# Optimization experiments

Measured on AMD Instinct MI355X. Metric: run time of the kernel, lower is better.

The kernel has to match this reference:

```python
import jax, jax.numpy as jnp
import numpy as np

B, S, W = 8, 1024, 512          # batch, bert seq len, max word num
D, H, F, L, V = 768, 12, 3072, 4, 28996
CH = 512                         # BERT_MAX_LEN chunk size
EPS = 1e-12

def _ln(x, g, b):
    mu = x.mean(-1, keepdims=True)
    var = ((x - mu) ** 2).mean(-1, keepdims=True)
    return (x - mu) / jnp.sqrt(var + EPS) * g + b

def setup_inputs() -> dict:
    key = jax.random.key(0)
    ks = jax.random.split(key, 32)
    s = 0.02
    inp = {}
    inp['x_bert'] = jax.random.randint(ks[0], (B, S), 0, V)
    inp['x_bert_mask'] = jnp.ones((B, S), jnp.float32)
    bnd = jnp.sort(jax.random.randint(ks[1], (B, W + 1), 0, S + 1), axis=1)
    inp['x_bert_offset'] = jnp.stack([bnd[:, :-1], bnd[:, 1:]], axis=-1)  # [B,W,2], st<=ed
    inp['x_mask'] = jax.random.randint(ks[2], (B, W), 0, 2).astype(jnp.int32)
    inp['word_emb'] = jax.random.normal(ks[3], (V, D), jnp.float32) * s
    inp['pos_emb'] = jax.random.normal(ks[4], (CH, D), jnp.float32) * s
    inp['type_emb'] = jax.random.normal(ks[5], (2, D), jnp.float32) * s
    inp['emb_g'] = jnp.ones((D,), jnp.float32); inp['emb_b'] = jnp.zeros((D,), jnp.float32)
    inp['Wq'] = jax.random.normal(ks[6], (L, D, D), jnp.float32) * s
    inp['bq'] = jnp.zeros((L, D), jnp.float32)
    inp['Wk'] = jax.random.normal(ks[7], (L, D, D), jnp.float32) * s
    inp['bk'] = jnp.zeros((L, D), jnp.float32)
    inp['Wv'] = jax.random.normal(ks[8], (L, D, D), jnp.float32) * s
    inp['bv'] = jnp.zeros((L, D), jnp.float32)
    inp['Wo'] = jax.random.normal(ks[9], (L, D, D), jnp.float32) * s
    inp['bo'] = jnp.zeros((L, D), jnp.float32)
    inp['ln1_g'] = jnp.ones((L, D), jnp.float32); inp['ln1_b'] = jnp.zeros((L, D), jnp.float32)
    inp['W1'] = jax.random.normal(ks[10], (L, D, F), jnp.float32) * s
    inp['b1f'] = jnp.zeros((L, F), jnp.float32)
    inp['W2'] = jax.random.normal(ks[11], (L, F, D), jnp.float32) * s
    inp['b2f'] = jnp.zeros((L, D), jnp.float32)
    inp['ln2_g'] = jnp.ones((L, D), jnp.float32); inp['ln2_b'] = jnp.zeros((L, D), jnp.float32)
    return inp

def reference(x_bert, x_bert_mask, x_bert_offset, x_mask, word_emb, pos_emb, type_emb,
              emb_g, emb_b, Wq, bq, Wk, bk, Wv, bv, Wo, bo, ln1_g, ln1_b,
              W1, b1f, W2, b2f, ln2_g, ln2_b):
    nch = S // CH
    # chunking the sequence into 512-token BERT calls == folding chunks into batch
    ids = x_bert.reshape(B * nch, CH)
    m = x_bert_mask.reshape(B * nch, CH)
    h = word_emb[ids] + pos_emb[None] + type_emb[0][None, None]
    h = _ln(h, emb_g, emb_b)
    bias = (1.0 - m)[:, None, None, :] * -10000.0  # HF-style extended attention mask
    dh = D // H
    scale = 1.0 / np.sqrt(dh).astype(np.float32)
    def layer(h, p):
        wq, bq_, wk, bk_, wv, bv_, wo, bo_, g1, be1, w1, bf1, w2, bf2, g2, be2 = p
        q = (h @ wq + bq_).reshape(-1, CH, H, dh)
        k = (h @ wk + bk_).reshape(-1, CH, H, dh)
        v = (h @ wv + bv_).reshape(-1, CH, H, dh)
        scores = jnp.einsum('bqhd,bkhd->bhqk', q, k) * scale + bias
        a = jax.nn.softmax(scores, axis=-1)
        ctx = jnp.einsum('bhqk,bkhd->bqhd', a, v).reshape(-1, CH, D)
        h1 = _ln(h + ctx @ wo + bo_, g1, be1)
        ff = jax.nn.gelu(h1 @ w1 + bf1, approximate=False) @ w2 + bf2
        h2 = _ln(h1 + ff, g2, be2)
        return h2, None
    h, _ = jax.lax.scan(layer, h, (Wq, bq, Wk, bk, Wv, bv, Wo, bo, ln1_g, ln1_b,
                                   W1, b1f, W2, b2f, ln2_g, ln2_b))
    emb = h.reshape(B, S, D)  # concat of chunk last_hidden_states
    # offset-based mean pooling via exclusive cumsum (single fused pass)
    cs = jnp.concatenate([jnp.zeros((B, 1, D), emb.dtype), jnp.cumsum(emb, axis=1)], axis=1)
    st = x_bert_offset[..., 0]
    ed = x_bert_offset[..., 1]
    gat = lambda idx: jnp.take_along_axis(cs, jnp.broadcast_to(idx[:, :, None], (B, W, D)), axis=1)
    sums = gat(ed) - gat(st)
    cnt = (ed - st).astype(emb.dtype)
    valid = (x_mask != 0) & (st < ed)
    out = jnp.where(valid[:, :, None], sums / jnp.maximum(cnt, 1.0)[:, :, None], 0.0)
    return out
```

## Files before the change

kernel.cpp:

```cpp
#include <hip/hip_runtime.h>
#include <hip/hip_bf16.h>


#define TOK   8192
#define DM    768
#define DQKV  2304
#define DF    3072
#define NPAIR 192
#define SCH   512

typedef __bf16 v8bf  __attribute__((ext_vector_type(8)));
typedef float  f32x4 __attribute__((ext_vector_type(4)));

__device__ __align__(256) float g_h   [TOK * DM];
__device__ __align__(256) float g_h1  [TOK * DM];
__device__ __align__(256) float g_tmp [TOK * DM];
__device__ __align__(256) short g_hb  [TOK * DM];
__device__ __align__(256) short g_h1b [TOK * DM];
__device__ __align__(256) short g_qkv [TOK * DQKV];
__device__ __align__(256) short g_ctxb[TOK * DM];
__device__ __align__(256) short g_ffb [TOK * DF];
__device__ __align__(256) short g_vt  [(size_t)NPAIR * 64 * SCH];
__device__ __align__(256) short g_sb  [(size_t)NPAIR * SCH * SCH];
__device__ __align__(256) short g_pb  [(size_t)NPAIR * SCH * SCH];
__device__ __align__(256) short g_wqkvT[4 * (size_t)DQKV * DM];
__device__ __align__(256) short g_woT  [4 * (size_t)DM * DM];
__device__ __align__(256) short g_w1T  [4 * (size_t)DF * DM];
__device__ __align__(256) short g_w2T  [4 * (size_t)DM * DF];
__device__ __align__(256) float g_bqkv [4 * DQKV];

__device__ __forceinline__ void g2l16(const short* g, short* l) {
    __builtin_amdgcn_global_load_lds(
        (const __attribute__((address_space(1))) void*)g,
        (__attribute__((address_space(3))) void*)l, 16, 0, 0);
}

__device__ inline float block_sum(float v, float* s4) {
#pragma unroll
    for (int o = 32; o > 0; o >>= 1) v += __shfl_down(v, o, 64);
    int lane = threadIdx.x & 63, w = threadIdx.x >> 6;
    __syncthreads();
    if (lane == 0) s4[w] = v;
    __syncthreads();
    return s4[0] + s4[1] + s4[2] + s4[3];
}

__global__ __launch_bounds__(256) void wconv(
    const float* __restrict__ in, short* __restrict__ out,
    int K, int N, long long inLS, long long outLS)
{
    in  += (size_t)blockIdx.z * inLS;
    out += (size_t)blockIdx.z * outLS;
    int k0 = blockIdx.y * 32, n0 = blockIdx.x * 32;
    __shared__ float s[32][33];
    int tr = threadIdx.x >> 5, tc = threadIdx.x & 31;
#pragma unroll
    for (int i = 0; i < 4; i++)
        s[tr + i * 8][tc] = in[(size_t)(k0 + tr + i * 8) * N + n0 + tc];
    __syncthreads();
    __hip_bfloat16* ob = (__hip_bfloat16*)out;
#pragma unroll
    for (int i = 0; i < 4; i++)
        ob[(size_t)(n0 + tr + i * 8) * K + k0 + tc] = __float2bfloat16(s[tc][tr + i * 8]);
}

__global__ __launch_bounds__(256) void concat_bias(
    const float* __restrict__ bq, const float* __restrict__ bk,
    const float* __restrict__ bv, float* __restrict__ out)
{
    int idx = blockIdx.x * 256 + threadIdx.x;
    if (idx >= 4 * DQKV) return;
    int l = idx / DQKV, n = idx % DQKV;
    float v = (n < 768) ? bq[l * 768 + n]
            : (n < 1536) ? bk[l * 768 + n - 768]
                         : bv[l * 768 + n - 1536];
    out[idx] = v;
}

__global__ __launch_bounds__(256) void embed_ln_kernel(
    const int* __restrict__ ids, const float* __restrict__ wemb,
    const float* __restrict__ pemb, const float* __restrict__ temb,
    const float* __restrict__ g, const float* __restrict__ b,
    float* __restrict__ outf, short* __restrict__ outb)
{
    int row = blockIdx.x;
    int pos = row & (SCH - 1);
    long id = ids[row];
    __shared__ float s4[4];
    float vals[3];
    float sum = 0.f;
#pragma unroll
    for (int i = 0; i < 3; i++) {
        int d = threadIdx.x + i * 256;
        float e = wemb[id * DM + d] + pemb[pos * DM + d] + temb[d];
        vals[i] = e; sum += e;
    }
    float mu = block_sum(sum, s4) * (1.f / DM);
    float vs = 0.f;
#pragma unroll
    for (int i = 0; i < 3; i++) { float t = vals[i] - mu; vs += t * t; }
    float rstd = rsqrtf(block_sum(vs, s4) * (1.f / DM) + 1e-12f);
    __hip_bfloat16* ob = (__hip_bfloat16*)outb;
#pragma unroll
    for (int i = 0; i < 3; i++) {
        int d = threadIdx.x + i * 256;
        float v = (vals[i] - mu) * rstd * g[d] + b[d];
        outf[(size_t)row * DM + d] = v;
        ob[(size_t)row * DM + d] = __float2bfloat16(v);
    }
}

__global__ __launch_bounds__(256) void add_ln_kernel(
    const float* __restrict__ x, const float* __restrict__ res,
    const float* __restrict__ g, const float* __restrict__ b,
    float* __restrict__ outf, short* __restrict__ outb)
{
    int row = blockIdx.x;
    const float* xr = x + (size_t)row * DM;
    const float* rr = res + (size_t)row * DM;
    __shared__ float s4[4];
    float vals[3];
    float sum = 0.f;
#pragma unroll
    for (int i = 0; i < 3; i++) {
        int d = threadIdx.x + i * 256;
        float e = xr[d] + rr[d];
        vals[i] = e; sum += e;
    }
    float mu = block_sum(sum, s4) * (1.f / DM);
    float vs = 0.f;
#pragma unroll
    for (int i = 0; i < 3; i++) { float t = vals[i] - mu; vs += t * t; }
    float rstd = rsqrtf(block_sum(vs, s4) * (1.f / DM) + 1e-12f);
    __hip_bfloat16* ob = (__hip_bfloat16*)outb;
#pragma unroll
    for (int i = 0; i < 3; i++) {
        int d = threadIdx.x + i * 256;
        float v = (vals[i] - mu) * rstd * g[d] + b[d];
        outf[(size_t)row * DM + d] = v;
        ob[(size_t)row * DM + d] = __float2bfloat16(v);
    }
}

template<int BM, int BN>
__global__ __launch_bounds__(256) void mfma_gemm(
    const short* __restrict__ A, int lda, long long sA1, long long sA2,
    const short* __restrict__ B, int ldb, long long sB1, long long sB2,
    const float* __restrict__ bias,
    float* __restrict__ Cf, short* __restrict__ Cb, int ldc,
    long long sC1, long long sC2, int bdiv, int K, int act)
{
    constexpr int WCOLS = BN / 64;
    __shared__ __align__(16) short As[BM * 64];
    __shared__ __align__(16) short Bs[BN * 64];

    int bz = blockIdx.z;
    long long zq = bz / bdiv, zr = bz % bdiv;
    A += zq * sA1 + zr * sA2;
    B += zq * sB1 + zr * sB2;
    const long long coff = zq * sC1 + zr * sC2;

    const int tid = threadIdx.x;
    const int w = tid >> 6, l = tid & 63;
    const int lr = l >> 3, lc = l & 7;
    const int lcs = lc ^ lr;
    const int quad = l >> 4, m16 = l & 15;
    const int wm0 = (w / WCOLS) * 64, wn0 = (w % WCOLS) * 64;
    const int row0 = blockIdx.y * BM, col0 = blockIdx.x * BN;

    f32x4 acc[4][4] = {};

    for (int k0 = 0; k0 < K; k0 += 64) {
#pragma unroll
        for (int i = 0; i < BM / 32; i++) {
            int ch = w * (BM / 32) + i;
            g2l16(A + (size_t)(row0 + ch * 8 + lr) * lda + k0 + lcs * 8,
                  As + ch * 512 + l * 8);
        }
#pragma unroll
        for (int i = 0; i < BN / 32; i++) {
            int ch = w * (BN / 32) + i;
            g2l16(B + (size_t)(col0 + ch * 8 + lr) * ldb + k0 + lcs * 8,
                  Bs + ch * 512 + l * 8);
        }
        __syncthreads();
#pragma unroll
        for (int ks = 0; ks < 2; ks++) {
            int g = ks * 4 + quad;
            v8bf af[4], bfr[4];
#pragma unroll
            for (int rb = 0; rb < 4; rb++) {
                int r = wm0 + rb * 16 + m16;
                af[rb] = *(const v8bf*)&As[r * 64 + ((g ^ (r & 7)) << 3)];
            }
#pragma unroll
            for (int cb = 0; cb < 4; cb++) {
                int r = wn0 + cb * 16 + m16;
                bfr[cb] = *(const v8bf*)&Bs[r * 64 + ((g ^ (r & 7)) << 3)];
            }
#pragma unroll
            for (int rb = 0; rb < 4; rb++)
#pragma unroll
                for (int cb = 0; cb < 4; cb++)
                    acc[rb][cb] = __builtin_amdgcn_mfma_f32_16x16x32_bf16(
                        af[rb], bfr[cb], acc[rb][cb], 0, 0, 0);
        }
        __syncthreads();
    }

    float* cf = Cf ? Cf + coff : nullptr;
    __hip_bfloat16* cbp = Cb ? (__hip_bfloat16*)Cb + coff : nullptr;
#pragma unroll
    for (int cb = 0; cb < 4; cb++) {
        int col = col0 + wn0 + cb * 16 + m16;
        float bvv = bias ? bias[col] : 0.f;
#pragma unroll
        for (int rb = 0; rb < 4; rb++) {
            int rbase = row0 + wm0 + rb * 16 + quad * 4;
#pragma unroll
            for (int r = 0; r < 4; r++) {
                float v = acc[rb][cb][r] + bvv;
                if (act) v = 0.5f * v * (1.f + erff(v * 0.70710678118654752f));
                size_t off = (size_t)(rbase + r) * ldc + col;
                if (cf) cf[off] = v;
                else    cbp[off] = __float2bfloat16(v);
            }
        }
    }
}

__global__ __launch_bounds__(256) void softmax_bf16(
    const short* __restrict__ sb, short* __restrict__ pb,
    const float* __restrict__ bmask)
{
    int w = threadIdx.x >> 6, l = threadIdx.x & 63;
    int r = blockIdx.x * 4 + w;
    int pair = r >> 9, row = r & 511;
    int chunk = pair / 12;
    size_t off = (size_t)pair * (SCH * SCH) + (size_t)row * SCH;
    const __hip_bfloat16* p = (const __hip_bfloat16*)sb + off;
    const float* mrow = bmask + chunk * SCH;
    float v[8];
    float mx = -1e30f;
#pragma unroll
    for (int i = 0; i < 8; i++) {
        int j = l + i * 64;
        v[i] = __bfloat162float(p[j]) * 0.125f + (1.f - mrow[j]) * (-10000.f);
        mx = fmaxf(mx, v[i]);
    }
#pragma unroll
    for (int o = 32; o > 0; o >>= 1) mx = fmaxf(mx, __shfl_down(mx, o, 64));
    mx = __shfl(mx, 0, 64);
    float s = 0.f;
#pragma unroll
    for (int i = 0; i < 8; i++) { v[i] = expf(v[i] - mx); s += v[i]; }
#pragma unroll
    for (int o = 32; o > 0; o >>= 1) s += __shfl_down(s, o, 64);
    s = __shfl(s, 0, 64);
    float inv = 1.f / s;
    __hip_bfloat16* q = (__hip_bfloat16*)pb + off;
#pragma unroll
    for (int i = 0; i < 8; i++) q[l + i * 64] = __float2bfloat16(v[i] * inv);
}

__global__ __launch_bounds__(256) void transpose_v(
    const short* __restrict__ qkv, short* __restrict__ vt)
{
    int pair = blockIdx.y, chunk = pair / 12, head = pair % 12;
    int t0 = blockIdx.x * 64;
    __shared__ short s[64][68];
    int tr = threadIdx.x >> 4;
    int tc = (threadIdx.x & 15) * 4;
    const short* src = qkv + 1536 + (size_t)(chunk * SCH + t0) * DQKV + head * 64;
#pragma unroll
    for (int i = 0; i < 4; i++) {
        int t = tr + i * 16;
        ushort4 u = *(const ushort4*)(src + (size_t)t * DQKV + tc);
        s[t][tc] = u.x; s[t][tc + 1] = u.y; s[t][tc + 2] = u.z; s[t][tc + 3] = u.w;
    }
    __syncthreads();
    short* dst = vt + (size_t)pair * 64 * SCH + t0;
#pragma unroll
    for (int i = 0; i < 4; i++) {
        int d = tr + i * 16;
        ushort4 o;
        o.x = s[tc][d]; o.y = s[tc + 1][d]; o.z = s[tc + 2][d]; o.w = s[tc + 3][d];
        *(ushort4*)(dst + (size_t)d * SCH + tc) = o;
    }
}

__global__ __launch_bounds__(256) void pool_kernel(
    const float* __restrict__ h, const int* __restrict__ offs,
    const int* __restrict__ wmask, float* __restrict__ out)
{
    int bw = blockIdx.x;
    int b = bw >> 9;
    int st = offs[bw * 2], ed = offs[bw * 2 + 1];
    bool valid = (wmask[bw] != 0) && (st < ed);
    float* orow = out + (size_t)bw * DM;
    float inv = valid ? 1.f / (float)(ed - st) : 0.f;
#pragma unroll
    for (int i = 0; i < 3; i++) {
        int d = threadIdx.x + i * 256;
        float s = 0.f;
        if (valid) {
            for (int t = st; t < ed; t++)
                s += h[((size_t)b * 1024 + t) * DM + d];
            s *= inv;
        }
        orow[d] = s;
    }
}

extern "C" void kernel_launch(void* const* d_in, const int* in_sizes, int n_in,
                              void* d_out, int out_size, void* d_ws, size_t ws_size,
                              hipStream_t stream) {
    const int*   x_bert   = (const int*)  d_in[0];
    const float* x_bmask  = (const float*)d_in[1];
    const int*   x_offset = (const int*)  d_in[2];
    const int*   x_wmask  = (const int*)  d_in[3];
    const float* wemb     = (const float*)d_in[4];
    const float* pemb     = (const float*)d_in[5];
    const float* temb     = (const float*)d_in[6];
    const float* emb_g    = (const float*)d_in[7];
    const float* emb_b    = (const float*)d_in[8];
    const float* Wq  = (const float*)d_in[9];
    const float* bq  = (const float*)d_in[10];
    const float* Wk  = (const float*)d_in[11];
    const float* bk  = (const float*)d_in[12];
    const float* Wv  = (const float*)d_in[13];
    const float* bv  = (const float*)d_in[14];
    const float* Wo  = (const float*)d_in[15];
    const float* bo  = (const float*)d_in[16];
    const float* ln1g = (const float*)d_in[17];
    const float* ln1b = (const float*)d_in[18];
    const float* W1  = (const float*)d_in[19];
    const float* b1f = (const float*)d_in[20];
    const float* W2  = (const float*)d_in[21];
    const float* b2f = (const float*)d_in[22];
    const float* ln2g = (const float*)d_in[23];
    const float* ln2b = (const float*)d_in[24];
    float* out = (float*)d_out;

    float *h, *h1, *tmp, *bqkv;
    short *hb, *h1b, *qkv, *ctxb, *ffb, *vt, *sb, *pb, *wqkvT, *woT, *w1T, *w2T;
    hipGetSymbolAddress((void**)&h,    HIP_SYMBOL(g_h));
    hipGetSymbolAddress((void**)&h1,   HIP_SYMBOL(g_h1));
    hipGetSymbolAddress((void**)&tmp,  HIP_SYMBOL(g_tmp));
    hipGetSymbolAddress((void**)&hb,   HIP_SYMBOL(g_hb));
    hipGetSymbolAddress((void**)&h1b,  HIP_SYMBOL(g_h1b));
    hipGetSymbolAddress((void**)&qkv,  HIP_SYMBOL(g_qkv));
    hipGetSymbolAddress((void**)&ctxb, HIP_SYMBOL(g_ctxb));
    hipGetSymbolAddress((void**)&ffb,  HIP_SYMBOL(g_ffb));
    hipGetSymbolAddress((void**)&vt,   HIP_SYMBOL(g_vt));
    hipGetSymbolAddress((void**)&sb,   HIP_SYMBOL(g_sb));
    hipGetSymbolAddress((void**)&pb,   HIP_SYMBOL(g_pb));
    hipGetSymbolAddress((void**)&wqkvT,HIP_SYMBOL(g_wqkvT));
    hipGetSymbolAddress((void**)&woT,  HIP_SYMBOL(g_woT));
    hipGetSymbolAddress((void**)&w1T,  HIP_SYMBOL(g_w1T));
    hipGetSymbolAddress((void**)&w2T,  HIP_SYMBOL(g_w2T));
    hipGetSymbolAddress((void**)&bqkv, HIP_SYMBOL(g_bqkv));

    dim3 wtA(DM / 32, DM / 32, 4);
    wconv<<<wtA, 256, 0, stream>>>(Wq, wqkvT,              DM, DM, (long long)DM * DM, (long long)DQKV * DM);
    wconv<<<wtA, 256, 0, stream>>>(Wk, wqkvT + 768 * DM,   DM, DM, (long long)DM * DM, (long long)DQKV * DM);
    wconv<<<wtA, 256, 0, stream>>>(Wv, wqkvT + 1536 * DM,  DM, DM, (long long)DM * DM, (long long)DQKV * DM);
    wconv<<<wtA, 256, 0, stream>>>(Wo, woT,                DM, DM, (long long)DM * DM, (long long)DM * DM);
    dim3 wtB(DF / 32, DM / 32, 4);
    wconv<<<wtB, 256, 0, stream>>>(W1, w1T, DM, DF, (long long)DM * DF, (long long)DF * DM);
    dim3 wtC(DM / 32, DF / 32, 4);
    wconv<<<wtC, 256, 0, stream>>>(W2, w2T, DF, DM, (long long)DF * DM, (long long)DM * DF);
    concat_bias<<<(4 * DQKV + 255) / 256, 256, 0, stream>>>(bq, bk, bv, bqkv);

    embed_ln_kernel<<<TOK, 256, 0, stream>>>(x_bert, wemb, pemb, temb, emb_g, emb_b, h, hb);

    const long long sQ1 = (long long)SCH * DQKV;
    const long long sS1 = 12LL * SCH * SCH;
    const long long sS2 = (long long)SCH * SCH;
    const long long sV1 = 12LL * 64 * SCH;
    const long long sV2 = 64LL * SCH;

    for (int l = 0; l < 4; l++) {
        const short* wqkvl = wqkvT + (size_t)l * DQKV * DM;
        const short* wol   = woT  + (size_t)l * DM * DM;
        const short* w1l   = w1T  + (size_t)l * DF * DM;
        const short* w2l   = w2T  + (size_t)l * DM * DF;

        mfma_gemm<128, 128><<<dim3(DQKV / 128, TOK / 128, 1), 256, 0, stream>>>(
            hb, DM, 0, 0, wqkvl, DM, 0, 0, bqkv + l * DQKV,
            nullptr, qkv, DQKV, 0, 0, 1, DM, 0);

        mfma_gemm<128, 128><<<dim3(4, 4, NPAIR), 256, 0, stream>>>(
            qkv,       DQKV, sQ1, 64,
            qkv + 768, DQKV, sQ1, 64,
            nullptr, nullptr, sb, SCH, sS1, sS2, 12, 64, 0);

        softmax_bf16<<<NPAIR * SCH / 4, 256, 0, stream>>>(sb, pb, x_bmask);

        transpose_v<<<dim3(8, NPAIR), 256, 0, stream>>>(qkv, vt);

        mfma_gemm<256, 64><<<dim3(1, 2, NPAIR), 256, 0, stream>>>(
            pb, SCH, sS1, sS2,
            vt, SCH, sV1, sV2,
            nullptr, nullptr, ctxb, DM, (long long)SCH * DM, 64, 12, SCH, 0);

        mfma_gemm<128, 128><<<dim3(DM / 128, TOK / 128, 1), 256, 0, stream>>>(
            ctxb, DM, 0, 0, wol, DM, 0, 0, bo + (size_t)l * DM,
            tmp, nullptr, DM, 0, 0, 1, DM, 0);
        add_ln_kernel<<<TOK, 256, 0, stream>>>(tmp, h, ln1g + (size_t)l * DM, ln1b + (size_t)l * DM, h1, h1b);

        mfma_gemm<128, 128><<<dim3(DF / 128, TOK / 128, 1), 256, 0, stream>>>(
            h1b, DM, 0, 0, w1l, DM, 0, 0, b1f + (size_t)l * DF,
            nullptr, ffb, DF, 0, 0, 1, DM, 1);
        mfma_gemm<128, 128><<<dim3(DM / 128, TOK / 128, 1), 256, 0, stream>>>(
            ffb, DF, 0, 0, w2l, DF, 0, 0, b2f + (size_t)l * DM,
            tmp, nullptr, DM, 0, 0, 1, DF, 0);
        add_ln_kernel<<<TOK, 256, 0, stream>>>(tmp, h1, ln2g + (size_t)l * DM, ln2b + (size_t)l * DM, h, hb);
    }

    pool_kernel<<<8 * 512, 256, 0, stream>>>(h, x_offset, x_wmask, out);
}
```

Before: 1.870 ms.

## Replace materialized attention with flash attention; double-buffer GEMM; fuse residual add

New measurement: 1.787 ms. -4.4%, faster.

```diff
diff --git a/kernel.cpp b/kernel.cpp
--- a/kernel.cpp
+++ b/kernel.cpp
@@ -21,8 +21,6 @@
 __device__ __align__(256) short g_ctxb[TOK * DM];
 __device__ __align__(256) short g_ffb [TOK * DF];
 __device__ __align__(256) short g_vt  [(size_t)NPAIR * 64 * SCH];
-__device__ __align__(256) short g_sb  [(size_t)NPAIR * SCH * SCH];
-__device__ __align__(256) short g_pb  [(size_t)NPAIR * SCH * SCH];
 __device__ __align__(256) short g_wqkvT[4 * (size_t)DQKV * DM];
 __device__ __align__(256) short g_woT  [4 * (size_t)DM * DM];
 __device__ __align__(256) short g_w1T  [4 * (size_t)DF * DM];
@@ -110,21 +108,20 @@
     }
 }
 
-__global__ __launch_bounds__(256) void add_ln_kernel(
-    const float* __restrict__ x, const float* __restrict__ res,
+__global__ __launch_bounds__(256) void ln_kernel(
+    const float* __restrict__ x,
     const float* __restrict__ g, const float* __restrict__ b,
     float* __restrict__ outf, short* __restrict__ outb)
 {
     int row = blockIdx.x;
     const float* xr = x + (size_t)row * DM;
-    const float* rr = res + (size_t)row * DM;
     __shared__ float s4[4];
     float vals[3];
     float sum = 0.f;
 #pragma unroll
     for (int i = 0; i < 3; i++) {
         int d = threadIdx.x + i * 256;
-        float e = xr[d] + rr[d];
+        float e = xr[d];
         vals[i] = e; sum += e;
     }
     float mu = block_sum(sum, s4) * (1.f / DM);
@@ -142,48 +139,47 @@
     }
 }
 
-template<int BM, int BN>
 __global__ __launch_bounds__(256) void mfma_gemm(
-    const short* __restrict__ A, int lda, long long sA1, long long sA2,
-    const short* __restrict__ B, int ldb, long long sB1, long long sB2,
-    const float* __restrict__ bias,
-    float* __restrict__ Cf, short* __restrict__ Cb, int ldc,
-    long long sC1, long long sC2, int bdiv, int K, int act)
-{
-    constexpr int WCOLS = BN / 64;
-    __shared__ __align__(16) short As[BM * 64];
-    __shared__ __align__(16) short Bs[BN * 64];
-
-    int bz = blockIdx.z;
-    long long zq = bz / bdiv, zr = bz % bdiv;
-    A += zq * sA1 + zr * sA2;
-    B += zq * sB1 + zr * sB2;
-    const long long coff = zq * sC1 + zr * sC2;
+    const short* __restrict__ A, int lda,
+    const short* __restrict__ B, int ldb,
+    const float* __restrict__ bias, const float* __restrict__ res,
+    float* __restrict__ Cf, short* __restrict__ Cb, int ldc, int K, int act)
+{
+    __shared__ __align__(16) short As[2][128 * 64];
+    __shared__ __align__(16) short Bs[2][128 * 64];
 
     const int tid = threadIdx.x;
     const int w = tid >> 6, l = tid & 63;
     const int lr = l >> 3, lc = l & 7;
     const int lcs = lc ^ lr;
     const int quad = l >> 4, m16 = l & 15;
-    const int wm0 = (w / WCOLS) * 64, wn0 = (w % WCOLS) * 64;
-    const int row0 = blockIdx.y * BM, col0 = blockIdx.x * BN;
+    const int wm0 = (w >> 1) * 64, wn0 = (w & 1) * 64;
+    const int row0 = blockIdx.y * 128, col0 = blockIdx.x * 128;
+
+    const short* Abase = A + (size_t)(row0 + lr) * lda + lcs * 8;
+    const short* Bbase = B + (size_t)(col0 + lr) * ldb + lcs * 8;
+
+    auto stage = [&](int k0, int buf) {
+#pragma unroll
+        for (int i = 0; i < 4; i++) {
+            int ch = w * 4 + i;
+            g2l16(Abase + (size_t)ch * 8 * lda + k0, &As[buf][ch * 512 + l * 8]);
+        }
+#pragma unroll
+        for (int i = 0; i < 4; i++) {
+            int ch = w * 4 + i;
+            g2l16(Bbase + (size_t)ch * 8 * ldb + k0, &Bs[buf][ch * 512 + l * 8]);
+        }
+    };
 
     f32x4 acc[4][4] = {};
-
-    for (int k0 = 0; k0 < K; k0 += 64) {
-#pragma unroll
-        for (int i = 0; i < BM / 32; i++) {
-            int ch = w * (BM / 32) + i;
-            g2l16(A + (size_t)(row0 + ch * 8 + lr) * lda + k0 + lcs * 8,
-                  As + ch * 512 + l * 8);
-        }
-#pragma unroll
-        for (int i = 0; i < BN / 32; i++) {
-            int ch = w * (BN / 32) + i;
-            g2l16(B + (size_t)(col0 + ch * 8 + lr) * ldb + k0 + lcs * 8,
-                  Bs + ch * 512 + l * 8);
-        }
+    stage(0, 0);
+    const int nk = K >> 6;
+    for (int kk = 0; kk < nk; kk++) {
         __syncthreads();
+        if (kk + 1 < nk) stage((kk + 1) << 6, (kk + 1) & 1);
+        const short* as = As[kk & 1];
+        const short* bs = Bs[kk & 1];
 #pragma unroll
         for (int ks = 0; ks < 2; ks++) {
             int g = ks * 4 + quad;
@@ -191,12 +187,12 @@
 #pragma unroll
             for (int rb = 0; rb < 4; rb++) {
                 int r = wm0 + rb * 16 + m16;
-                af[rb] = *(const v8bf*)&As[r * 64 + ((g ^ (r & 7)) << 3)];
+                af[rb] = *(const v8bf*)&as[r * 64 + ((g ^ (r & 7)) << 3)];
             }
 #pragma unroll
             for (int cb = 0; cb < 4; cb++) {
                 int r = wn0 + cb * 16 + m16;
-                bfr[cb] = *(const v8bf*)&Bs[r * 64 + ((g ^ (r & 7)) << 3)];
+                bfr[cb] = *(const v8bf*)&bs[r * 64 + ((g ^ (r & 7)) << 3)];
             }
 #pragma unroll
             for (int rb = 0; rb < 4; rb++)
@@ -205,11 +201,9 @@
                     acc[rb][cb] = __builtin_amdgcn_mfma_f32_16x16x32_bf16(
                         af[rb], bfr[cb], acc[rb][cb], 0, 0, 0);
         }
-        __syncthreads();
-    }
-
-    float* cf = Cf ? Cf + coff : nullptr;
-    __hip_bfloat16* cbp = Cb ? (__hip_bfloat16*)Cb + coff : nullptr;
+    }
+
+    __hip_bfloat16* cbp = (__hip_bfloat16*)Cb;
 #pragma unroll
     for (int cb = 0; cb < 4; cb++) {
         int col = col0 + wn0 + cb * 16 + m16;
@@ -219,48 +213,179 @@
             int rbase = row0 + wm0 + rb * 16 + quad * 4;
 #pragma unroll
             for (int r = 0; r < 4; r++) {
+                size_t off = (size_t)(rbase + r) * ldc + col;
                 float v = acc[rb][cb][r] + bvv;
                 if (act) v = 0.5f * v * (1.f + erff(v * 0.70710678118654752f));
-                size_t off = (size_t)(rbase + r) * ldc + col;
-                if (cf) cf[off] = v;
+                if (res) v += res[off];
+                if (Cf) Cf[off] = v;
                 else    cbp[off] = __float2bfloat16(v);
             }
         }
     }
 }
 
-__global__ __launch_bounds__(256) void softmax_bf16(
-    const short* __restrict__ sb, short* __restrict__ pb,
-    const float* __restrict__ bmask)
-{
-    int w = threadIdx.x >> 6, l = threadIdx.x & 63;
-    int r = blockIdx.x * 4 + w;
-    int pair = r >> 9, row = r & 511;
-    int chunk = pair / 12;
-    size_t off = (size_t)pair * (SCH * SCH) + (size_t)row * SCH;
-    const __hip_bfloat16* p = (const __hip_bfloat16*)sb + off;
+__global__ __launch_bounds__(256) void flash_attn(
+    const short* __restrict__ qkv, const short* __restrict__ vt,
+    const float* __restrict__ bmask, short* __restrict__ ctxb)
+{
+    __shared__ __align__(16) short Kt[64 * 64];
+    __shared__ __align__(16) short Vt[64 * 64];
+    __shared__ __align__(16) short Pt[128 * 64];
+
+    const int pair = blockIdx.y, chunk = pair / 12, head = pair % 12;
+    const int q0 = blockIdx.x * 128;
+    const int tid = threadIdx.x;
+    const int w = tid >> 6, l = tid & 63;
+    const int lr = l >> 3, lc = l & 7, lcs = lc ^ lr;
+    const int quad = l >> 4, m16 = l & 15;
+
+    const short* Qbase = qkv + (size_t)(chunk * SCH + q0) * DQKV + head * 64;
+    const short* Kbase = qkv + 768 + (size_t)(chunk * SCH) * DQKV + head * 64;
+    const short* Vbase = vt + (size_t)pair * 64 * SCH;
     const float* mrow = bmask + chunk * SCH;
-    float v[8];
-    float mx = -1e30f;
-#pragma unroll
-    for (int i = 0; i < 8; i++) {
-        int j = l + i * 64;
-        v[i] = __bfloat162float(p[j]) * 0.125f + (1.f - mrow[j]) * (-10000.f);
-        mx = fmaxf(mx, v[i]);
-    }
-#pragma unroll
-    for (int o = 32; o > 0; o >>= 1) mx = fmaxf(mx, __shfl_down(mx, o, 64));
-    mx = __shfl(mx, 0, 64);
-    float s = 0.f;
-#pragma unroll
-    for (int i = 0; i < 8; i++) { v[i] = expf(v[i] - mx); s += v[i]; }
-#pragma unroll
-    for (int o = 32; o > 0; o >>= 1) s += __shfl_down(s, o, 64);
-    s = __shfl(s, 0, 64);
-    float inv = 1.f / s;
-    __hip_bfloat16* q = (__hip_bfloat16*)pb + off;
-#pragma unroll
-    for (int i = 0; i < 8; i++) q[l + i * 64] = __float2bfloat16(v[i] * inv);
+
+#pragma unroll
+    for (int i = 0; i < 4; i++) {
+        int ch = w * 4 + i;
+        g2l16(Qbase + (size_t)(ch * 8 + lr) * DQKV + lcs * 8, &Pt[ch * 512 + l * 8]);
+    }
+    __syncthreads();
+    v8bf qf[2][2];
+#pragma unroll
+    for (int rb = 0; rb < 2; rb++) {
+        int r = w * 32 + rb * 16 + m16;
+#pragma unroll
+        for (int ks = 0; ks < 2; ks++) {
+            int g = ks * 4 + quad;
+            qf[rb][ks] = *(const v8bf*)&Pt[r * 64 + ((g ^ (r & 7)) << 3)];
+        }
+    }
+
+    f32x4 accO[2][4] = {};
+    float m_i[2][4], l_i[2][4];
+#pragma unroll
+    for (int rb = 0; rb < 2; rb++)
+#pragma unroll
+        for (int r = 0; r < 4; r++) { m_i[rb][r] = -1e30f; l_i[rb][r] = 0.f; }
+
+    for (int t0 = 0; t0 < SCH; t0 += 64) {
+        __syncthreads();
+#pragma unroll
+        for (int i = 0; i < 2; i++) {
+            int ch = w * 2 + i;
+            g2l16(Kbase + (size_t)(t0 + ch * 8 + lr) * DQKV + lcs * 8,
+                  &Kt[ch * 512 + l * 8]);
+            g2l16(Vbase + (size_t)(ch * 8 + lr) * SCH + t0 + lcs * 8,
+                  &Vt[ch * 512 + l * 8]);
+        }
+        __syncthreads();
+
+        float mb[4];
+#pragma unroll
+        for (int cb = 0; cb < 4; cb++)
+            mb[cb] = (1.f - mrow[t0 + cb * 16 + m16]) * -10000.f;
+
+        f32x4 accS[2][4] = {};
+#pragma unroll
+        for (int ks = 0; ks < 2; ks++) {
+            int g = ks * 4 + quad;
+            v8bf kf[4];
+#pragma unroll
+            for (int cb = 0; cb < 4; cb++) {
+                int r = cb * 16 + m16;
+                kf[cb] = *(const v8bf*)&Kt[r * 64 + ((g ^ (r & 7)) << 3)];
+            }
+#pragma unroll
+            for (int rb = 0; rb < 2; rb++)
+#pragma unroll
+                for (int cb = 0; cb < 4; cb++)
+                    accS[rb][cb] = __builtin_amdgcn_mfma_f32_16x16x32_bf16(
+                        qf[rb][ks], kf[cb], accS[rb][cb], 0, 0, 0);
+        }
+
+#pragma unroll
+        for (int rb = 0; rb < 2; rb++) {
+#pragma unroll
+            for (int r = 0; r < 4; r++) {
+                float mx = -1e30f;
+#pragma unroll
+                for (int cb = 0; cb < 4; cb++) {
+                    float sv = accS[rb][cb][r] * 0.125f + mb[cb];
+                    accS[rb][cb][r] = sv;
+                    mx = fmaxf(mx, sv);
+                }
+#pragma unroll
+                for (int x = 1; x < 16; x <<= 1)
+                    mx = fmaxf(mx, __shfl_xor(mx, x, 64));
+                float mnew = fmaxf(m_i[rb][r], mx);
+                float alpha = expf(m_i[rb][r] - mnew);
+                m_i[rb][r] = mnew;
+                float rs = 0.f;
+#pragma unroll
+                for (int cb = 0; cb < 4; cb++) {
+                    float p = expf(accS[rb][cb][r] - mnew);
+                    accS[rb][cb][r] = p;
+                    rs += p;
+                }
+#pragma unroll
+                for (int x = 1; x < 16; x <<= 1)
+                    rs += __shfl_xor(rs, x, 64);
+                l_i[rb][r] = l_i[rb][r] * alpha + rs;
+#pragma unroll
+                for (int cb = 0; cb < 4; cb++)
+                    accO[rb][cb][r] *= alpha;
+            }
+        }
+
+        __hip_bfloat16* ptb = (__hip_bfloat16*)Pt;
+#pragma unroll
+        for (int rb = 0; rb < 2; rb++)
+#pragma unroll
+            for (int cb = 0; cb < 4; cb++) {
+                int kg = cb * 2 + (m16 >> 3), j = m16 & 7;
+#pragma unroll
+                for (int r = 0; r < 4; r++) {
+                    int row = w * 32 + rb * 16 + quad * 4 + r;
+                    ptb[row * 64 + ((kg ^ (row & 7)) << 3) + j] =
+                        __float2bfloat16(accS[rb][cb][r]);
+                }
+            }
+
+#pragma unroll
+        for (int ks = 0; ks < 2; ks++) {
+            int g = ks * 4 + quad;
+            v8bf vf[4], pf[2];
+#pragma unroll
+            for (int cb = 0; cb < 4; cb++) {
+                int r = cb * 16 + m16;
+                vf[cb] = *(const v8bf*)&Vt[r * 64 + ((g ^ (r & 7)) << 3)];
+            }
+#pragma unroll
+            for (int rb = 0; rb < 2; rb++) {
+                int r = w * 32 + rb * 16 + m16;
+                pf[rb] = *(const v8bf*)&Pt[r * 64 + ((g ^ (r & 7)) << 3)];
+            }
+#pragma unroll
+            for (int rb = 0; rb < 2; rb++)
+#pragma unroll
+                for (int cb = 0; cb < 4; cb++)
+                    accO[rb][cb] = __builtin_amdgcn_mfma_f32_16x16x32_bf16(
+                        pf[rb], vf[cb], accO[rb][cb], 0, 0, 0);
+        }
+    }
+
+    __hip_bfloat16* ob = (__hip_bfloat16*)ctxb;
+#pragma unroll
+    for (int rb = 0; rb < 2; rb++)
+#pragma unroll
+        for (int r = 0; r < 4; r++) {
+            int row = q0 + w * 32 + rb * 16 + quad * 4 + r;
+            float inv = 1.f / l_i[rb][r];
+            size_t base = (size_t)(chunk * SCH + row) * DM + head * 64;
+#pragma unroll
+            for (int cb = 0; cb < 4; cb++)
+                ob[base + cb * 16 + m16] = __float2bfloat16(accO[rb][cb][r] * inv);
+        }
 }
 
 __global__ __launch_bounds__(256) void transpose_v(
@@ -343,7 +468,7 @@
     float* out = (float*)d_out;
 
     float *h, *h1, *tmp, *bqkv;
-    short *hb, *h1b, *qkv, *ctxb, *ffb, *vt, *sb, *pb, *wqkvT, *woT, *w1T, *w2T;
+    short *hb, *h1b, *qkv, *ctxb, *ffb, *vt, *wqkvT, *woT, *w1T, *w2T;
     hipGetSymbolAddress((void**)&h,    HIP_SYMBOL(g_h));
     hipGetSymbolAddress((void**)&h1,   HIP_SYMBOL(g_h1));
     hipGetSymbolAddress((void**)&tmp,  HIP_SYMBOL(g_tmp));
@@ -353,8 +478,6 @@
     hipGetSymbolAddress((void**)&ctxb, HIP_SYMBOL(g_ctxb));
     hipGetSymbolAddress((void**)&ffb,  HIP_SYMBOL(g_ffb));
     hipGetSymbolAddress((void**)&vt,   HIP_SYMBOL(g_vt));
-    hipGetSymbolAddress((void**)&sb,   HIP_SYMBOL(g_sb));
-    hipGetSymbolAddress((void**)&pb,   HIP_SYMBOL(g_pb));
     hipGetSymbolAddress((void**)&wqkvT,HIP_SYMBOL(g_wqkvT));
     hipGetSymbolAddress((void**)&woT,  HIP_SYMBOL(g_woT));
     hipGetSymbolAddress((void**)&w1T,  HIP_SYMBOL(g_w1T));
@@ -362,10 +485,10 @@
     hipGetSymbolAddress((void**)&bqkv, HIP_SYMBOL(g_bqkv));
 
     dim3 wtA(DM / 32, DM / 32, 4);
-    wconv<<<wtA, 256, 0, stream>>>(Wq, wqkvT,              DM, DM, (long long)DM * DM, (long long)DQKV * DM);
-    wconv<<<wtA, 256, 0, stream>>>(Wk, wqkvT + 768 * DM,   DM, DM, (long long)DM * DM, (long long)DQKV * DM);
-    wconv<<<wtA, 256, 0, stream>>>(Wv, wqkvT + 1536 * DM,  DM, DM, (long long)DM * DM, (long long)DQKV * DM);
-    wconv<<<wtA, 256, 0, stream>>>(Wo, woT,                DM, DM, (long long)DM * DM, (long long)DM * DM);
+    wconv<<<wtA, 256, 0, stream>>>(Wq, wqkvT,             DM, DM, (long long)DM * DM, (long long)DQKV * DM);
+    wconv<<<wtA, 256, 0, stream>>>(Wk, wqkvT + 768 * DM,  DM, DM, (long long)DM * DM, (long long)DQKV * DM);
+    wconv<<<wtA, 256, 0, stream>>>(Wv, wqkvT + 1536 * DM, DM, DM, (long long)DM * DM, (long long)DQKV * DM);
+    wconv<<<wtA, 256, 0, stream>>>(Wo, woT,               DM, DM, (long long)DM * DM, (long long)DM * DM);
     dim3 wtB(DF / 32, DM / 32, 4);
     wconv<<<wtB, 256, 0, stream>>>(W1, w1T, DM, DF, (long long)DM * DF, (long long)DF * DM);
     dim3 wtC(DM / 32, DF / 32, 4);
@@ -374,48 +497,32 @@
 
     embed_ln_kernel<<<TOK, 256, 0, stream>>>(x_bert, wemb, pemb, temb, emb_g, emb_b, h, hb);
 
-    const long long sQ1 = (long long)SCH * DQKV;
-    const long long sS1 = 12LL * SCH * SCH;
-    const long long sS2 = (long long)SCH * SCH;
-    const long long sV1 = 12LL * 64 * SCH;
-    const long long sV2 = 64LL * SCH;
-
     for (int l = 0; l < 4; l++) {
         const short* wqkvl = wqkvT + (size_t)l * DQKV * DM;
         const short* wol   = woT  + (size_t)l * DM * DM;
         const short* w1l   = w1T  + (size_t)l * DF * DM;
         const short* w2l   = w2T  + (size_t)l * DM * DF;
 
-        mfma_gemm<128, 128><<<dim3(DQKV / 128, TOK / 128, 1), 256, 0, stream>>>(
-            hb, DM, 0, 0, wqkvl, DM, 0, 0, bqkv + l * DQKV,
-            nullptr, qkv, DQKV, 0, 0, 1, DM, 0);
-
-        mfma_gemm<128, 128><<<dim3(4, 4, NPAIR), 256, 0, stream>>>(
-            qkv,       DQKV, sQ1, 64,
-            qkv + 768, DQKV, sQ1, 64,
-            nullptr, nullptr, sb, SCH, sS1, sS2, 12, 64, 0);
-
-        softmax_bf16<<<NPAIR * SCH / 4, 256, 0, stream>>>(sb, pb, x_bmask);
+        mfma_gemm<<<dim3(DQKV / 128, TOK / 128), 256, 0, stream>>>(
+            hb, DM, wqkvl, DM, bqkv + l * DQKV, nullptr,
+            nullptr, qkv, DQKV, DM, 0);
 
         transpose_v<<<dim3(8, NPAIR), 256, 0, stream>>>(qkv, vt);
 
-        mfma_gemm<256, 64><<<dim3(1, 2, NPAIR), 256, 0, stream>>>(
-            pb, SCH, sS1, sS2,
-            vt, SCH, sV1, sV2,
-            nullptr, nullptr, ctxb, DM, (long long)SCH * DM, 64, 12, SCH, 0);
-
-        mfma_gemm<128, 128><<<dim3(DM / 128, TOK / 128, 1), 256, 0, stream>>>(
-            ctxb, DM, 0, 0, wol, DM, 0, 0, bo + (size_t)l * DM,
-            tmp, nullptr, DM, 0, 0, 1, DM, 0);
-        add_ln_kernel<<<TOK, 256, 0, stream>>>(tmp, h, ln1g + (size_t)l * DM, ln1b + (size_t)l * DM, h1, h1b);
-
-        mfma_gemm<128, 128><<<dim3(DF / 128, TOK / 128, 1), 256, 0, stream>>>(
-            h1b, DM, 0, 0, w1l, DM, 0, 0, b1f + (size_t)l * DF,
-            nullptr, ffb, DF, 0, 0, 1, DM, 1);
-        mfma_gemm<128, 128><<<dim3(DM / 128, TOK / 128, 1), 256, 0, stream>>>(
-            ffb, DF, 0, 0, w2l, DF, 0, 0, b2f + (size_t)l * DM,
-            tmp, nullptr, DM, 0, 0, 1, DF, 0);
-        add_ln_kernel<<<TOK, 256, 0, stream>>>(tmp, h1, ln2g + (size_t)l * DM, ln2b + (size_t)l * DM, h, hb);
+        flash_attn<<<dim3(4, NPAIR), 256, 0, stream>>>(qkv, vt, x_bmask, ctxb);
+
+        mfma_gemm<<<dim3(DM / 128, TOK / 128), 256, 0, stream>>>(
+            ctxb, DM, wol, DM, bo + (size_t)l * DM, h,
+            tmp, nullptr, DM, DM, 0);
+        ln_kernel<<<TOK, 256, 0, stream>>>(tmp, ln1g + (size_t)l * DM, ln1b + (size_t)l * DM, h1, h1b);
+
+        mfma_gemm<<<dim3(DF / 128, TOK / 128), 256, 0, stream>>>(
+            h1b, DM, w1l, DM, b1f + (size_t)l * DF, nullptr,
+            nullptr, ffb, DF, DM, 1);
+        mfma_gemm<<<dim3(DM / 128, TOK / 128), 256, 0, stream>>>(
+            ffb, DF, w2l, DF, b2f + (size_t)l * DM, h1,
+            tmp, nullptr, DM, DF, 0);
+        ln_kernel<<<TOK, 256, 0, stream>>>(tmp, ln2g + (size_t)l * DM, ln2b + (size_t)l * DM, h, hb);
     }
 
     pool_kernel<<<8 * 512, 256, 0, stream>>>(h, x_offset, x_wmask, out);
```
